# Kernel optimization log

Hardware: AMD Instinct MI355X
Metric: run time of the kernel (lower is better)

Reference implementation:

```python
import jax, jax.numpy as jnp
import numpy as np

T = 32  # simulation_length
L = 4   # number of NeuralCores in the chain


def to_uniform_spikes(x, cycle, sim_len):
    """Uniform spike encoding: emit round(x*T) spikes evenly spaced over T cycles.
    Faithful to SpikingUnifiedCoreFlow.to_uniform_spikes."""
    N = jnp.round(x * sim_len).astype(jnp.int32)
    mask = (N != 0) & (N != sim_len) & (cycle < sim_len)
    N_safe = jnp.maximum(N, 1)
    spacing = sim_len / N_safe.astype(x.dtype)          # T / N
    fire = mask & (jnp.floor(cycle / spacing) < N_safe) & (jnp.floor(jnp.mod(cycle, spacing)) == 0)
    out = fire.astype(x.dtype)
    return jnp.where(N == sim_len, jnp.ones_like(out), out)  # saturated channels fire every cycle


def setup_inputs() -> dict:
    key = jax.random.key(0)
    k0, k1 = jax.random.split(key)
    x = jax.random.uniform(k0, (128, 1024), dtype=jnp.float32)          # activations in [0,1]
    weights = jax.random.normal(k1, (L, 1024, 1024), dtype=jnp.float32) * 0.02  # (neurons, axons) per core
    thresholds = jnp.ones((L,), dtype=jnp.float32)
    return {"x": x, "weights": weights, "thresholds": thresholds}


def reference(x, weights, thresholds):
    """Rate-mode spiking simulation over a chain of NeuralCores.
    Per cycle: encode input to spikes (Uniform), propagate through cores with
    LIF integration (membrane += W @ spikes; spike = threshold < membrane;
    membrane -= spike * threshold), output = mean spike train of last core."""
    B = x.shape[0]
    H = weights.shape[1]

    def step(mem, cycle):
        sig = to_uniform_spikes(x, cycle, T)            # (B, axons_in)
        new_mems = []
        for l in range(L):
            m = mem[l] + sig @ weights[l].T             # F.linear(sig, W)
            s = (thresholds[l] < m).astype(x.dtype)     # thresholding_mode '<'
            m = m - s * thresholds[l]                   # Default firing: subtract reset
            new_mems.append(m)
            sig = s                                     # feed downstream core this cycle
        return jnp.stack(new_mems), sig                 # sig = last core spikes

    mem0 = jnp.zeros((L, B, H), dtype=x.dtype)
    _, out_spikes = jax.lax.scan(step, mem0, jnp.arange(T))  # (T, B, H)
    return out_spikes.mean(axis=0)                      # spike counts -> rates
```

## Files before the change

kernel.cpp:

```cpp
#include <hip/hip_runtime.h>
#include <stdint.h>


typedef __attribute__((ext_vector_type(4)))  int   i32x4;
typedef __attribute__((ext_vector_type(16))) int   i32x16;
typedef __attribute__((ext_vector_type(4)))  float f32x4;

#define SCALE_F 4294967296.0f
#define NSL 4

__device__ __forceinline__ void gload16(const void* g, void* l) {
    __builtin_amdgcn_global_load_lds(
        (const __attribute__((address_space(1))) void*)g,
        (__attribute__((address_space(3))) void*)l, 16, 0, 0);
}

__device__ __forceinline__ i32x4 expand16(unsigned int f) {
    i32x4 r;
    #pragma unroll
    for (int d = 0; d < 4; ++d)
        r[d] = (int)((((f >> (4 * d)) & 0xFu) * 0x00204081u) & 0x01010101u);
    return r;
}

__global__ void k_prep(const float* __restrict__ x, const float* __restrict__ w,
                       uint32_t* __restrict__ Am, signed char* __restrict__ planes) {
    if (blockIdx.x < 4096) {
        int tid = blockIdx.x * 256 + threadIdx.x;
        int l = tid >> 18;
        int rest4 = (tid & 0x3FFFF) << 2;
        f32x4 wv = *reinterpret_cast<const f32x4*>(w + ((size_t)l << 20) + rest4);
        long long q[4];
        #pragma unroll
        for (int i = 0; i < 4; ++i) q[i] = llrintf(wv[i] * SCALE_F);
        #pragma unroll
        for (int s = 0; s < NSL; ++s) {
            uint32_t pack = 0;
            #pragma unroll
            for (int i = 0; i < 4; ++i) {
                int d = (int)(signed char)((unsigned char)(q[i] & 255));
                q[i] = (q[i] - d) >> 8;
                pack |= ((uint32_t)(unsigned char)d) << (8 * i);
            }
            *reinterpret_cast<uint32_t*>(planes + (((size_t)(l * NSL + s)) << 20) + rest4) = pack;
        }
    } else {
        const int wid  = ((blockIdx.x - 4096) * 256 + threadIdx.x) >> 6;
        const int lane = threadIdx.x & 63;
        const int b = wid >> 4, kc = wid & 15;
        float v = x[b * 1024 + kc * 64 + lane];
        int N = (int)rintf(v * 32.0f);
        uint32_t bits = 0;
        if (N >= 32) {
            bits = 0xFFFFFFFFu;
        } else if (N > 0) {
            float spacing = 32.0f / (float)N;
            #pragma unroll
            for (int t = 0; t < 32; ++t) {
                float fm = fmodf((float)t, spacing);
                if (fm < 1.0f) bits |= (1u << t);
            }
        }
        uint32_t cap = 0;
        #pragma unroll
        for (int t = 0; t < 32; ++t) {
            unsigned long long bal = __ballot((bits >> t) & 1u);
            if (lane == t)      cap = (uint32_t)bal;
            if (lane == t + 32) cap = (uint32_t)(bal >> 32);
        }
        const int t = lane & 31, ww = lane >> 5;
        Am[(size_t)(b * 32 + t) * 32 + kc * 2 + ww] = cap;
    }
}

__global__ __launch_bounds__(512, 4) void k_fused(
        const uint32_t* __restrict__ Am,
        const signed char* __restrict__ planes,
        const float* __restrict__ th,
        uint32_t* __restrict__ AmNext,
        float* __restrict__ out,
        int layer) {
    __shared__ alignas(16) signed char lds[2][32768];

    const int tid  = threadIdx.x;
    const int lane = tid & 63;
    const int wave = tid >> 6;
    const int mw   = wave >> 1;
    const int nw   = wave & 1;
    const int lr   = lane & 31;
    const int hi   = lane >> 5;

    const int xc = blockIdx.x & 7, q = blockIdx.x >> 3;
    const int nTile = xc * 2 + (q & 1);
    const int mTile = q >> 1;
    const int mBase = mTile * 128, nBase = nTile * 64;

    const signed char* srcB[NSL];
    {
        const int r0 = tid >> 3, qs = tid & 7;
        const int sw0 = (qs ^ (r0 & 7)) * 16;
        #pragma unroll
        for (int s = 0; s < NSL; ++s)
            srcB[s] = planes + (((size_t)(layer * NSL + s)) << 20)
                    + (size_t)(nBase + r0) * 1024 + sw0;
    }
    const uint32_t* aRow = Am + (size_t)(mBase + mw * 32 + lr) * 32;

    int baddr[4];
    {
        const int brow = nw * 32 + lr;
        #pragma unroll
        for (int ks = 0; ks < 4; ++ks)
            baddr[ks] = brow * 128 + (((ks * 2 + hi) ^ (brow & 7)) * 16);
    }

    i32x16 acc[NSL];
    #pragma unroll
    for (int s = 0; s < NSL; ++s)
        #pragma unroll
        for (int r = 0; r < 16; ++r) acc[s][r] = 0;

    auto H0 = [&](int buf, int c) {
        const int ko = c * 128;
        gload16(srcB[0] + ko, &lds[buf][0]    + tid * 16);
        gload16(srcB[1] + ko, &lds[buf][8192] + tid * 16);
    };
    auto H1 = [&](int buf, int c) {
        const int ko = c * 128;
        gload16(srcB[2] + ko, &lds[buf][16384] + tid * 16);
        gload16(srcB[3] + ko, &lds[buf][24576] + tid * 16);
    };

    i32x4 amr[2];
    H0(0, 0);
    amr[0] = *reinterpret_cast<const i32x4*>(aRow);
    H1(0, 0);

    #pragma unroll
    for (int c = 0; c < 8; ++c) {
        const int buf = c & 1;
        const signed char* lb = &lds[buf][0];

        asm volatile("s_waitcnt vmcnt(2)" ::: "memory");
        __builtin_amdgcn_s_barrier();
        asm volatile("" ::: "memory");

        if (c + 1 < 8) {
            H0(buf ^ 1, c + 1);
            amr[(c + 1) & 1] = *reinterpret_cast<const i32x4*>(aRow + (c + 1) * 4);
            H1(buf ^ 1, c + 1);
        }

        i32x4 af[4];
        __builtin_amdgcn_s_setprio(1);
        #pragma unroll
        for (int ks = 0; ks < 4; ++ks) {
            af[ks] = expand16((((unsigned)amr[c & 1][ks]) >> (16 * hi)) & 0xFFFFu);
            #pragma unroll
            for (int s = 0; s < 2; ++s) {
                i32x4 bf = *reinterpret_cast<const i32x4*>(lb + s * 8192 + baddr[ks]);
                acc[s] = __builtin_amdgcn_mfma_i32_32x32x32_i8(af[ks], bf, acc[s], 0, 0, 0);
            }
        }
        __builtin_amdgcn_s_setprio(0);

        if (c + 1 < 8) asm volatile("s_waitcnt vmcnt(5)" ::: "memory");
        else           asm volatile("s_waitcnt vmcnt(0)" ::: "memory");
        __builtin_amdgcn_s_barrier();
        asm volatile("" ::: "memory");

        __builtin_amdgcn_s_setprio(1);
        #pragma unroll
        for (int ks = 0; ks < 4; ++ks) {
            #pragma unroll
            for (int s = 0; s < 2; ++s) {
                i32x4 bf = *reinterpret_cast<const i32x4*>(lb + (2 + s) * 8192 + baddr[ks]);
                acc[2 + s] = __builtin_amdgcn_mfma_i32_32x32x32_i8(af[ks], bf, acc[2 + s], 0, 0, 0);
            }
        }
        __builtin_amdgcn_s_setprio(0);
    }

    const long long TH = llrintf(th[layer] * SCALE_F);
    const int batch = mTile * 4 + mw;
    uint32_t bits = 0;
    long long mmem = 0;
    #pragma unroll
    for (int half = 0; half < 2; ++half) {
        long long own[8], par[8];
        #pragma unroll
        for (int r = 0; r < 8; ++r) {
            long long v = 0;
            #pragma unroll
            for (int s = 0; s < NSL; ++s)
                v += ((long long)acc[s][half * 8 + r]) << (8 * s);
            own[r] = v;
        }
        #pragma unroll
        for (int r = 0; r < 8; ++r) {
            int plo = __shfl((int)(uint32_t)own[r], lane ^ 32, 64);
            int phi = __shfl((int)(own[r] >> 32), lane ^ 32, 64);
            par[r] = ((long long)phi << 32) | (uint32_t)plo;
        }
        #pragma unroll
        for (int tq = 0; tq < 16; ++tq) {
            const int idx = (tq >> 3) * 4 + (tq & 3);
            const int usePar = ((tq >> 2) & 1) ^ hi;
            long long v = usePar ? par[idx] : own[idx];
            mmem += v;
            if (mmem > TH) { mmem -= TH; bits |= (1u << (half * 16 + tq)); }
        }
    }

    if (AmNext) {
        uint32_t cap = 0;
        #pragma unroll
        for (int t = 0; t < 32; ++t) {
            unsigned long long bal = __ballot((bits >> t) & 1u);
            if (lane == t) cap = (uint32_t)bal;
        }
        if (hi == 0)
            AmNext[(size_t)(batch * 32 + lr) * 32 + nTile * 2 + nw] = cap;
    } else if (hi == 0) {
        out[batch * 1024 + nBase + nw * 32 + lr] = (float)__popc(bits) * 0.03125f;
    }
}

extern "C" void kernel_launch(void* const* d_in, const int* in_sizes, int n_in,
                              void* d_out, int out_size, void* d_ws, size_t ws_size,
                              hipStream_t stream) {
    const float* x  = (const float*)d_in[0];
    const float* w  = (const float*)d_in[1];
    const float* th = (const float*)d_in[2];
    float* out = (float*)d_out;
    char* ws = (char*)d_ws;

    signed char* planes = (signed char*)(ws);
    uint32_t*    Am0    = (uint32_t*)(ws + 16777216);
    uint32_t*    Am1    = (uint32_t*)(ws + 17301504);

    k_prep<<<4608, 256, 0, stream>>>(x, w, Am0, planes);

    uint32_t* Ain = Am0;
    uint32_t* Anx = Am1;
    for (int l = 0; l < 4; ++l) {
        k_fused<<<512, 512, 0, stream>>>(Ain, planes, th,
                                         (l < 3) ? Anx : nullptr,
                                         (l == 3) ? out : nullptr, l);
        uint32_t* tmp = Ain; Ain = Anx; Anx = tmp;
    }
}
```

Before: 105.0 us.

## Register-block two M tiles per wave and halve block size in fused layer kernel

Blocks shrink from 8 to 4 waves. Each wave now computes two 32-row M tiles, so every B fragment read from LDS feeds two MFMAs. Each thread issues twice as many global-to-LDS loads, and the vmcnt waits are rescaled to the new load count per stage. This cuts LDS read traffic per MFMA and per-block overhead, at the cost of doubled accumulator registers and half as many waves per CU for latency hiding.

```diff
diff --git a/kernel.cpp b/kernel.cpp
--- a/kernel.cpp
+++ b/kernel.cpp
@@ -73,7 +73,7 @@
     }
 }
 
-__global__ __launch_bounds__(512, 4) void k_fused(
+__global__ __launch_bounds__(256, 2) void k_fused(
         const uint32_t* __restrict__ Am,
         const signed char* __restrict__ planes,
         const float* __restrict__ th,
@@ -104,7 +104,8 @@
             srcB[s] = planes + (((size_t)(layer * NSL + s)) << 20)
                     + (size_t)(nBase + r0) * 1024 + sw0;
     }
-    const uint32_t* aRow = Am + (size_t)(mBase + mw * 32 + lr) * 32;
+    const uint32_t* aRow0 = Am + (size_t)(mBase + mw * 64 + lr) * 32;
+    const uint32_t* aRow1 = aRow0 + 32 * 32;
 
     int baddr[4];
     {
@@ -114,26 +115,33 @@
             baddr[ks] = brow * 128 + (((ks * 2 + hi) ^ (brow & 7)) * 16);
     }
 
-    i32x16 acc[NSL];
-    #pragma unroll
-    for (int s = 0; s < NSL; ++s)
-        #pragma unroll
-        for (int r = 0; r < 16; ++r) acc[s][r] = 0;
+    i32x16 acc[2][NSL];
+    #pragma unroll
+    for (int m = 0; m < 2; ++m)
+        #pragma unroll
+        for (int s = 0; s < NSL; ++s)
+            #pragma unroll
+            for (int r = 0; r < 16; ++r) acc[m][s][r] = 0;
 
     auto H0 = [&](int buf, int c) {
         const int ko = c * 128;
-        gload16(srcB[0] + ko, &lds[buf][0]    + tid * 16);
-        gload16(srcB[1] + ko, &lds[buf][8192] + tid * 16);
+        gload16(srcB[0] + ko,         &lds[buf][0]     + tid * 16);
+        gload16(srcB[0] + ko + 32768, &lds[buf][4096]  + tid * 16);
+        gload16(srcB[1] + ko,         &lds[buf][8192]  + tid * 16);
+        gload16(srcB[1] + ko + 32768, &lds[buf][12288] + tid * 16);
     };
     auto H1 = [&](int buf, int c) {
         const int ko = c * 128;
-        gload16(srcB[2] + ko, &lds[buf][16384] + tid * 16);
-        gload16(srcB[3] + ko, &lds[buf][24576] + tid * 16);
+        gload16(srcB[2] + ko,         &lds[buf][16384] + tid * 16);
+        gload16(srcB[2] + ko + 32768, &lds[buf][20480] + tid * 16);
+        gload16(srcB[3] + ko,         &lds[buf][24576] + tid * 16);
+        gload16(srcB[3] + ko + 32768, &lds[buf][28672] + tid * 16);
     };
 
-    i32x4 amr[2];
+    i32x4 amr0[2], amr1[2];
     H0(0, 0);
-    amr[0] = *reinterpret_cast<const i32x4*>(aRow);
+    amr0[0] = *reinterpret_cast<const i32x4*>(aRow0);
+    amr1[0] = *reinterpret_cast<const i32x4*>(aRow1);
     H1(0, 0);
 
     #pragma unroll
@@ -141,30 +149,33 @@
         const int buf = c & 1;
         const signed char* lb = &lds[buf][0];
 
-        asm volatile("s_waitcnt vmcnt(2)" ::: "memory");
+        asm volatile("s_waitcnt vmcnt(4)" ::: "memory");
         __builtin_amdgcn_s_barrier();
         asm volatile("" ::: "memory");
 
         if (c + 1 < 8) {
             H0(buf ^ 1, c + 1);
-            amr[(c + 1) & 1] = *reinterpret_cast<const i32x4*>(aRow + (c + 1) * 4);
+            amr0[(c + 1) & 1] = *reinterpret_cast<const i32x4*>(aRow0 + (c + 1) * 4);
+            amr1[(c + 1) & 1] = *reinterpret_cast<const i32x4*>(aRow1 + (c + 1) * 4);
             H1(buf ^ 1, c + 1);
         }
 
-        i32x4 af[4];
+        i32x4 af0[4], af1[4];
         __builtin_amdgcn_s_setprio(1);
         #pragma unroll
         for (int ks = 0; ks < 4; ++ks) {
-            af[ks] = expand16((((unsigned)amr[c & 1][ks]) >> (16 * hi)) & 0xFFFFu);
-            #pragma unroll
-            for (int s = 0; s < 2; ++s) {
-                i32x4 bf = *reinterpret_cast<const i32x4*>(lb + s * 8192 + baddr[ks]);
-                acc[s] = __builtin_amdgcn_mfma_i32_32x32x32_i8(af[ks], bf, acc[s], 0, 0, 0);
-            }
+            af0[ks] = expand16((((unsigned)amr0[c & 1][ks]) >> (16 * hi)) & 0xFFFFu);
+            af1[ks] = expand16((((unsigned)amr1[c & 1][ks]) >> (16 * hi)) & 0xFFFFu);
+            i32x4 bf0 = *reinterpret_cast<const i32x4*>(lb + 0 * 8192 + baddr[ks]);
+            i32x4 bf1 = *reinterpret_cast<const i32x4*>(lb + 1 * 8192 + baddr[ks]);
+            acc[0][0] = __builtin_amdgcn_mfma_i32_32x32x32_i8(af0[ks], bf0, acc[0][0], 0, 0, 0);
+            acc[1][0] = __builtin_amdgcn_mfma_i32_32x32x32_i8(af1[ks], bf0, acc[1][0], 0, 0, 0);
+            acc[0][1] = __builtin_amdgcn_mfma_i32_32x32x32_i8(af0[ks], bf1, acc[0][1], 0, 0, 0);
+            acc[1][1] = __builtin_amdgcn_mfma_i32_32x32x32_i8(af1[ks], bf1, acc[1][1], 0, 0, 0);
         }
         __builtin_amdgcn_s_setprio(0);
 
-        if (c + 1 < 8) asm volatile("s_waitcnt vmcnt(5)" ::: "memory");
+        if (c + 1 < 8) asm volatile("s_waitcnt vmcnt(10)" ::: "memory");
         else           asm volatile("s_waitcnt vmcnt(0)" ::: "memory");
         __builtin_amdgcn_s_barrier();
         asm volatile("" ::: "memory");
@@ -172,57 +183,61 @@
         __builtin_amdgcn_s_setprio(1);
         #pragma unroll
         for (int ks = 0; ks < 4; ++ks) {
-            #pragma unroll
-            for (int s = 0; s < 2; ++s) {
-                i32x4 bf = *reinterpret_cast<const i32x4*>(lb + (2 + s) * 8192 + baddr[ks]);
-                acc[2 + s] = __builtin_amdgcn_mfma_i32_32x32x32_i8(af[ks], bf, acc[2 + s], 0, 0, 0);
-            }
+            i32x4 bf2 = *reinterpret_cast<const i32x4*>(lb + 2 * 8192 + baddr[ks]);
+            i32x4 bf3 = *reinterpret_cast<const i32x4*>(lb + 3 * 8192 + baddr[ks]);
+            acc[0][2] = __builtin_amdgcn_mfma_i32_32x32x32_i8(af0[ks], bf2, acc[0][2], 0, 0, 0);
+            acc[1][2] = __builtin_amdgcn_mfma_i32_32x32x32_i8(af1[ks], bf2, acc[1][2], 0, 0, 0);
+            acc[0][3] = __builtin_amdgcn_mfma_i32_32x32x32_i8(af0[ks], bf3, acc[0][3], 0, 0, 0);
+            acc[1][3] = __builtin_amdgcn_mfma_i32_32x32x32_i8(af1[ks], bf3, acc[1][3], 0, 0, 0);
         }
         __builtin_amdgcn_s_setprio(0);
     }
 
     const long long TH = llrintf(th[layer] * SCALE_F);
-    const int batch = mTile * 4 + mw;
-    uint32_t bits = 0;
-    long long mmem = 0;
-    #pragma unroll
-    for (int half = 0; half < 2; ++half) {
-        long long own[8], par[8];
-        #pragma unroll
-        for (int r = 0; r < 8; ++r) {
-            long long v = 0;
-            #pragma unroll
-            for (int s = 0; s < NSL; ++s)
-                v += ((long long)acc[s][half * 8 + r]) << (8 * s);
-            own[r] = v;
-        }
-        #pragma unroll
-        for (int r = 0; r < 8; ++r) {
-            int plo = __shfl((int)(uint32_t)own[r], lane ^ 32, 64);
-            int phi = __shfl((int)(own[r] >> 32), lane ^ 32, 64);
-            par[r] = ((long long)phi << 32) | (uint32_t)plo;
-        }
-        #pragma unroll
-        for (int tq = 0; tq < 16; ++tq) {
-            const int idx = (tq >> 3) * 4 + (tq & 3);
-            const int usePar = ((tq >> 2) & 1) ^ hi;
-            long long v = usePar ? par[idx] : own[idx];
-            mmem += v;
-            if (mmem > TH) { mmem -= TH; bits |= (1u << (half * 16 + tq)); }
-        }
-    }
-
-    if (AmNext) {
-        uint32_t cap = 0;
-        #pragma unroll
-        for (int t = 0; t < 32; ++t) {
-            unsigned long long bal = __ballot((bits >> t) & 1u);
-            if (lane == t) cap = (uint32_t)bal;
-        }
-        if (hi == 0)
-            AmNext[(size_t)(batch * 32 + lr) * 32 + nTile * 2 + nw] = cap;
-    } else if (hi == 0) {
-        out[batch * 1024 + nBase + nw * 32 + lr] = (float)__popc(bits) * 0.03125f;
+    #pragma unroll
+    for (int m = 0; m < 2; ++m) {
+        const int batch = mTile * 4 + mw * 2 + m;
+        uint32_t bits = 0;
+        long long mmem = 0;
+        #pragma unroll
+        for (int half = 0; half < 2; ++half) {
+            long long own[8], par[8];
+            #pragma unroll
+            for (int r = 0; r < 8; ++r) {
+                long long v = 0;
+                #pragma unroll
+                for (int s = 0; s < NSL; ++s)
+                    v += ((long long)acc[m][s][half * 8 + r]) << (8 * s);
+                own[r] = v;
+            }
+            #pragma unroll
+            for (int r = 0; r < 8; ++r) {
+                int plo = __shfl((int)(uint32_t)own[r], lane ^ 32, 64);
+                int phi = __shfl((int)(own[r] >> 32), lane ^ 32, 64);
+                par[r] = ((long long)phi << 32) | (uint32_t)plo;
+            }
+            #pragma unroll
+            for (int tq = 0; tq < 16; ++tq) {
+                const int idx = (tq >> 3) * 4 + (tq & 3);
+                const int usePar = ((tq >> 2) & 1) ^ hi;
+                long long v = usePar ? par[idx] : own[idx];
+                mmem += v;
+                if (mmem > TH) { mmem -= TH; bits |= (1u << (half * 16 + tq)); }
+            }
+        }
+
+        if (AmNext) {
+            uint32_t cap = 0;
+            #pragma unroll
+            for (int t = 0; t < 32; ++t) {
+                unsigned long long bal = __ballot((bits >> t) & 1u);
+                if (lane == t) cap = (uint32_t)bal;
+            }
+            if (hi == 0)
+                AmNext[(size_t)(batch * 32 + lr) * 32 + nTile * 2 + nw] = cap;
+        } else if (hi == 0) {
+            out[batch * 1024 + nBase + nw * 32 + lr] = (float)__popc(bits) * 0.03125f;
+        }
     }
 }
 
@@ -244,7 +259,7 @@
     uint32_t* Ain = Am0;
     uint32_t* Anx = Am1;
     for (int l = 0; l < 4; ++l) {
-        k_fused<<<512, 512, 0, stream>>>(Ain, planes, th,
+        k_fused<<<512, 256, 0, stream>>>(Ain, planes, th,
                                          (l < 3) ? Anx : nullptr,
                                          (l == 3) ? out : nullptr, l);
         uint32_t* tmp = Ain; Ain = Anx; Anx = tmp;
```

After: 105.0 us. Within noise of the previous version (+0.1%).

## Fuse four layer launches into one persistent kernel with grid barrier

Applied to the files above, without the earlier changes.

Replaces the four per-layer kernel launches with one persistent kernel that loops over layers and synchronises all 512 blocks through an atomic-counter grid barrier. The next layer's first weight-plane tile is prefetched into LDS before the barrier, so it overlaps the spike epilogue and the wait. This removes the launch gaps and kernel-boundary drains between layers. In exchange it assumes all 512 blocks are co-resident, or the spin barrier deadlocks. It also adds spinning atomic traffic and leaves AmIn un-qualified by restrict.

```diff
diff --git a/kernel.cpp b/kernel.cpp
--- a/kernel.cpp
+++ b/kernel.cpp
@@ -24,7 +24,9 @@
 }
 
 __global__ void k_prep(const float* __restrict__ x, const float* __restrict__ w,
-                       uint32_t* __restrict__ Am, signed char* __restrict__ planes) {
+                       uint32_t* __restrict__ Am, signed char* __restrict__ planes,
+                       unsigned* __restrict__ bar) {
+    if (blockIdx.x == 0 && threadIdx.x == 0) *bar = 0;
     if (blockIdx.x < 4096) {
         int tid = blockIdx.x * 256 + threadIdx.x;
         int l = tid >> 18;
@@ -73,13 +75,22 @@
     }
 }
 
-__global__ __launch_bounds__(512, 4) void k_fused(
-        const uint32_t* __restrict__ Am,
+__device__ __forceinline__ void grid_sync(unsigned* bar, unsigned target) {
+    __syncthreads();
+    if (threadIdx.x == 0) {
+        __hip_atomic_fetch_add(bar, 1u, __ATOMIC_RELEASE, __HIP_MEMORY_SCOPE_AGENT);
+        while (__hip_atomic_load(bar, __ATOMIC_ACQUIRE, __HIP_MEMORY_SCOPE_AGENT) < target)
+            __builtin_amdgcn_s_sleep(2);
+    }
+    __syncthreads();
+}
+
+__global__ __launch_bounds__(512, 4) void k_fused_all(
         const signed char* __restrict__ planes,
         const float* __restrict__ th,
-        uint32_t* __restrict__ AmNext,
+        uint32_t* Am0, uint32_t* Am1,
         float* __restrict__ out,
-        int layer) {
+        unsigned* __restrict__ bar) {
     __shared__ alignas(16) signed char lds[2][32768];
 
     const int tid  = threadIdx.x;
@@ -101,10 +112,9 @@
         const int sw0 = (qs ^ (r0 & 7)) * 16;
         #pragma unroll
         for (int s = 0; s < NSL; ++s)
-            srcB[s] = planes + (((size_t)(layer * NSL + s)) << 20)
+            srcB[s] = planes + ((size_t)s << 20)
                     + (size_t)(nBase + r0) * 1024 + sw0;
     }
-    const uint32_t* aRow = Am + (size_t)(mBase + mw * 32 + lr) * 32;
 
     int baddr[4];
     {
@@ -113,12 +123,6 @@
         for (int ks = 0; ks < 4; ++ks)
             baddr[ks] = brow * 128 + (((ks * 2 + hi) ^ (brow & 7)) * 16);
     }
-
-    i32x16 acc[NSL];
-    #pragma unroll
-    for (int s = 0; s < NSL; ++s)
-        #pragma unroll
-        for (int r = 0; r < 16; ++r) acc[s][r] = 0;
 
     auto H0 = [&](int buf, int c) {
         const int ko = c * 128;
@@ -131,98 +135,121 @@
         gload16(srcB[3] + ko, &lds[buf][24576] + tid * 16);
     };
 
-    i32x4 amr[2];
-    H0(0, 0);
-    amr[0] = *reinterpret_cast<const i32x4*>(aRow);
-    H1(0, 0);
-
-    #pragma unroll
-    for (int c = 0; c < 8; ++c) {
-        const int buf = c & 1;
-        const signed char* lb = &lds[buf][0];
-
-        asm volatile("s_waitcnt vmcnt(2)" ::: "memory");
-        __builtin_amdgcn_s_barrier();
-        asm volatile("" ::: "memory");
-
-        if (c + 1 < 8) {
-            H0(buf ^ 1, c + 1);
-            amr[(c + 1) & 1] = *reinterpret_cast<const i32x4*>(aRow + (c + 1) * 4);
-            H1(buf ^ 1, c + 1);
-        }
-
-        i32x4 af[4];
-        __builtin_amdgcn_s_setprio(1);
-        #pragma unroll
-        for (int ks = 0; ks < 4; ++ks) {
-            af[ks] = expand16((((unsigned)amr[c & 1][ks]) >> (16 * hi)) & 0xFFFFu);
-            #pragma unroll
-            for (int s = 0; s < 2; ++s) {
-                i32x4 bf = *reinterpret_cast<const i32x4*>(lb + s * 8192 + baddr[ks]);
-                acc[s] = __builtin_amdgcn_mfma_i32_32x32x32_i8(af[ks], bf, acc[s], 0, 0, 0);
-            }
-        }
-        __builtin_amdgcn_s_setprio(0);
-
-        if (c + 1 < 8) asm volatile("s_waitcnt vmcnt(5)" ::: "memory");
-        else           asm volatile("s_waitcnt vmcnt(0)" ::: "memory");
-        __builtin_amdgcn_s_barrier();
-        asm volatile("" ::: "memory");
-
-        __builtin_amdgcn_s_setprio(1);
-        #pragma unroll
-        for (int ks = 0; ks < 4; ++ks) {
-            #pragma unroll
-            for (int s = 0; s < 2; ++s) {
-                i32x4 bf = *reinterpret_cast<const i32x4*>(lb + (2 + s) * 8192 + baddr[ks]);
-                acc[2 + s] = __builtin_amdgcn_mfma_i32_32x32x32_i8(af[ks], bf, acc[2 + s], 0, 0, 0);
-            }
-        }
-        __builtin_amdgcn_s_setprio(0);
-    }
-
-    const long long TH = llrintf(th[layer] * SCALE_F);
-    const int batch = mTile * 4 + mw;
-    uint32_t bits = 0;
-    long long mmem = 0;
-    #pragma unroll
-    for (int half = 0; half < 2; ++half) {
-        long long own[8], par[8];
-        #pragma unroll
-        for (int r = 0; r < 8; ++r) {
-            long long v = 0;
-            #pragma unroll
-            for (int s = 0; s < NSL; ++s)
-                v += ((long long)acc[s][half * 8 + r]) << (8 * s);
-            own[r] = v;
-        }
-        #pragma unroll
-        for (int r = 0; r < 8; ++r) {
-            int plo = __shfl((int)(uint32_t)own[r], lane ^ 32, 64);
-            int phi = __shfl((int)(own[r] >> 32), lane ^ 32, 64);
-            par[r] = ((long long)phi << 32) | (uint32_t)plo;
-        }
-        #pragma unroll
-        for (int tq = 0; tq < 16; ++tq) {
-            const int idx = (tq >> 3) * 4 + (tq & 3);
-            const int usePar = ((tq >> 2) & 1) ^ hi;
-            long long v = usePar ? par[idx] : own[idx];
-            mmem += v;
-            if (mmem > TH) { mmem -= TH; bits |= (1u << (half * 16 + tq)); }
-        }
-    }
-
-    if (AmNext) {
-        uint32_t cap = 0;
-        #pragma unroll
-        for (int t = 0; t < 32; ++t) {
-            unsigned long long bal = __ballot((bits >> t) & 1u);
-            if (lane == t) cap = (uint32_t)bal;
-        }
-        if (hi == 0)
-            AmNext[(size_t)(batch * 32 + lr) * 32 + nTile * 2 + nw] = cap;
-    } else if (hi == 0) {
-        out[batch * 1024 + nBase + nw * 32 + lr] = (float)__popc(bits) * 0.03125f;
+    uint32_t* AmIn  = Am0;
+    uint32_t* AmOut = Am1;
+
+    #pragma unroll 1
+    for (int layer = 0; layer < 4; ++layer) {
+        const uint32_t* aRow = AmIn + (size_t)(mBase + mw * 32 + lr) * 32;
+
+        if (layer == 0) H0(0, 0);
+        i32x4 amr[2];
+        amr[0] = *reinterpret_cast<const i32x4*>(aRow);
+        H1(0, 0);
+
+        i32x16 acc[NSL];
+        #pragma unroll
+        for (int s = 0; s < NSL; ++s)
+            #pragma unroll
+            for (int r = 0; r < 16; ++r) acc[s][r] = 0;
+
+        #pragma unroll
+        for (int c = 0; c < 8; ++c) {
+            const int buf = c & 1;
+            const signed char* lb = &lds[buf][0];
+
+            asm volatile("s_waitcnt vmcnt(2)" ::: "memory");
+            __builtin_amdgcn_s_barrier();
+            asm volatile("" ::: "memory");
+
+            if (c + 1 < 8) {
+                H0(buf ^ 1, c + 1);
+                amr[(c + 1) & 1] = *reinterpret_cast<const i32x4*>(aRow + (c + 1) * 4);
+                H1(buf ^ 1, c + 1);
+            }
+
+            i32x4 af[4];
+            __builtin_amdgcn_s_setprio(1);
+            #pragma unroll
+            for (int ks = 0; ks < 4; ++ks) {
+                af[ks] = expand16((((unsigned)amr[c & 1][ks]) >> (16 * hi)) & 0xFFFFu);
+                #pragma unroll
+                for (int s = 0; s < 2; ++s) {
+                    i32x4 bf = *reinterpret_cast<const i32x4*>(lb + s * 8192 + baddr[ks]);
+                    acc[s] = __builtin_amdgcn_mfma_i32_32x32x32_i8(af[ks], bf, acc[s], 0, 0, 0);
+                }
+            }
+            __builtin_amdgcn_s_setprio(0);
+
+            if (c + 1 < 8) asm volatile("s_waitcnt vmcnt(5)" ::: "memory");
+            else           asm volatile("s_waitcnt vmcnt(0)" ::: "memory");
+            __builtin_amdgcn_s_barrier();
+            asm volatile("" ::: "memory");
+
+            __builtin_amdgcn_s_setprio(1);
+            #pragma unroll
+            for (int ks = 0; ks < 4; ++ks) {
+                #pragma unroll
+                for (int s = 0; s < 2; ++s) {
+                    i32x4 bf = *reinterpret_cast<const i32x4*>(lb + (2 + s) * 8192 + baddr[ks]);
+                    acc[2 + s] = __builtin_amdgcn_mfma_i32_32x32x32_i8(af[ks], bf, acc[2 + s], 0, 0, 0);
+                }
+            }
+            __builtin_amdgcn_s_setprio(0);
+        }
+
+        if (layer < 3) {
+            #pragma unroll
+            for (int s = 0; s < NSL; ++s) srcB[s] += (size_t)NSL << 20;
+            H0(0, 0);
+        }
+
+        const long long TH = llrintf(th[layer] * SCALE_F);
+        const int batch = mTile * 4 + mw;
+        uint32_t bits = 0;
+        long long mmem = 0;
+        #pragma unroll
+        for (int half = 0; half < 2; ++half) {
+            long long own[8], par[8];
+            #pragma unroll
+            for (int r = 0; r < 8; ++r) {
+                long long v = 0;
+                #pragma unroll
+                for (int s = 0; s < NSL; ++s)
+                    v += ((long long)acc[s][half * 8 + r]) << (8 * s);
+                own[r] = v;
+            }
+            #pragma unroll
+            for (int r = 0; r < 8; ++r) {
+                int plo = __shfl((int)(uint32_t)own[r], lane ^ 32, 64);
+                int phi = __shfl((int)(own[r] >> 32), lane ^ 32, 64);
+                par[r] = ((long long)phi << 32) | (uint32_t)plo;
+            }
+            #pragma unroll
+            for (int tq = 0; tq < 16; ++tq) {
+                const int idx = (tq >> 3) * 4 + (tq & 3);
+                const int usePar = ((tq >> 2) & 1) ^ hi;
+                long long v = usePar ? par[idx] : own[idx];
+                mmem += v;
+                if (mmem > TH) { mmem -= TH; bits |= (1u << (half * 16 + tq)); }
+            }
+        }
+
+        if (layer < 3) {
+            uint32_t cap = 0;
+            #pragma unroll
+            for (int t = 0; t < 32; ++t) {
+                unsigned long long bal = __ballot((bits >> t) & 1u);
+                if (lane == t) cap = (uint32_t)bal;
+            }
+            if (hi == 0)
+                AmOut[(size_t)(batch * 32 + lr) * 32 + nTile * 2 + nw] = cap;
+
+            grid_sync(bar, 512u * (unsigned)(layer + 1));
+            uint32_t* tmp = AmIn; AmIn = AmOut; AmOut = tmp;
+        } else if (hi == 0) {
+            out[batch * 1024 + nBase + nw * 32 + lr] = (float)__popc(bits) * 0.03125f;
+        }
     }
 }
 
@@ -238,15 +265,8 @@
     signed char* planes = (signed char*)(ws);
     uint32_t*    Am0    = (uint32_t*)(ws + 16777216);
     uint32_t*    Am1    = (uint32_t*)(ws + 17301504);
-
-    k_prep<<<4608, 256, 0, stream>>>(x, w, Am0, planes);
-
-    uint32_t* Ain = Am0;
-    uint32_t* Anx = Am1;
-    for (int l = 0; l < 4; ++l) {
-        k_fused<<<512, 512, 0, stream>>>(Ain, planes, th,
-                                         (l < 3) ? Anx : nullptr,
-                                         (l == 3) ? out : nullptr, l);
-        uint32_t* tmp = Ain; Ain = Anx; Anx = tmp;
-    }
-}
+    unsigned*    bar    = (unsigned*)(ws + 17825792);
+
+    k_prep<<<4608, 256, 0, stream>>>(x, w, Am0, planes, bar);
+    k_fused_all<<<512, 512, 0, stream>>>(planes, th, Am0, Am1, out, bar);
+}
```

Measured after the change: 221.6 us. 2.11x slower.

## Store weight byte-planes in k-chunk-major layout for conflict-free LDS reads

Applied to the files above, without the earlier changes.

The prep kernel now has each thread quantize 16 consecutive weights and write 16-byte packed groups into a layout where each 16-byte k-group is stored contiguously across all rows (g*16384 + row*16). The fused GEMM kernel's global-to-LDS loads and LDS read addresses are changed to match, replacing the XOR swizzle with plain k-group-major addressing. The aim is fewer, wider prep stores and simpler LDS addressing that stays free of bank conflicts. In exchange, each global load in the GEMM now strides 128 KB between chunks, and prep loads fewer but wider vectors per thread.

```diff
diff --git a/kernel.cpp b/kernel.cpp
--- a/kernel.cpp
+++ b/kernel.cpp
@@ -25,27 +25,42 @@
 
 __global__ void k_prep(const float* __restrict__ x, const float* __restrict__ w,
                        uint32_t* __restrict__ Am, signed char* __restrict__ planes) {
-    if (blockIdx.x < 4096) {
+    if (blockIdx.x < 1024) {
         int tid = blockIdx.x * 256 + threadIdx.x;
-        int l = tid >> 18;
-        int rest4 = (tid & 0x3FFFF) << 2;
-        f32x4 wv = *reinterpret_cast<const f32x4*>(w + ((size_t)l << 20) + rest4);
-        long long q[4];
-        #pragma unroll
-        for (int i = 0; i < 4; ++i) q[i] = llrintf(wv[i] * SCALE_F);
+        int l    = tid >> 16;
+        int rest = tid & 0xFFFF;
+        int row  = rest >> 6;
+        int g    = rest & 63;
+        const float* wp = w + ((size_t)l << 20) + (size_t)row * 1024 + g * 16;
+        long long q[16];
+        #pragma unroll
+        for (int i = 0; i < 16; i += 4) {
+            f32x4 wv = *reinterpret_cast<const f32x4*>(wp + i);
+            q[i + 0] = llrintf(wv[0] * SCALE_F);
+            q[i + 1] = llrintf(wv[1] * SCALE_F);
+            q[i + 2] = llrintf(wv[2] * SCALE_F);
+            q[i + 3] = llrintf(wv[3] * SCALE_F);
+        }
         #pragma unroll
         for (int s = 0; s < NSL; ++s) {
-            uint32_t pack = 0;
-            #pragma unroll
-            for (int i = 0; i < 4; ++i) {
-                int d = (int)(signed char)((unsigned char)(q[i] & 255));
-                q[i] = (q[i] - d) >> 8;
-                pack |= ((uint32_t)(unsigned char)d) << (8 * i);
-            }
-            *reinterpret_cast<uint32_t*>(planes + (((size_t)(l * NSL + s)) << 20) + rest4) = pack;
+            i32x4 pk;
+            #pragma unroll
+            for (int e = 0; e < 4; ++e) {
+                uint32_t pack = 0;
+                #pragma unroll
+                for (int i = 0; i < 4; ++i) {
+                    int idx = e * 4 + i;
+                    int d = (int)(signed char)((unsigned char)(q[idx] & 255));
+                    q[idx] = (q[idx] - d) >> 8;
+                    pack |= ((uint32_t)(unsigned char)d) << (8 * i);
+                }
+                pk[e] = (int)pack;
+            }
+            *reinterpret_cast<i32x4*>(planes + (((size_t)(l * NSL + s)) << 20)
+                                      + (size_t)g * 16384 + row * 16) = pk;
         }
     } else {
-        const int wid  = ((blockIdx.x - 4096) * 256 + threadIdx.x) >> 6;
+        const int wid  = ((blockIdx.x - 1024) * 256 + threadIdx.x) >> 6;
         const int lane = threadIdx.x & 63;
         const int b = wid >> 4, kc = wid & 15;
         float v = x[b * 1024 + kc * 64 + lane];
@@ -97,12 +112,12 @@
 
     const signed char* srcB[NSL];
     {
-        const int r0 = tid >> 3, qs = tid & 7;
-        const int sw0 = (qs ^ (r0 & 7)) * 16;
+        const int ks0 = tid >> 6;
+        const int rr  = tid & 63;
         #pragma unroll
         for (int s = 0; s < NSL; ++s)
             srcB[s] = planes + (((size_t)(layer * NSL + s)) << 20)
-                    + (size_t)(nBase + r0) * 1024 + sw0;
+                    + (size_t)ks0 * 16384 + (size_t)(nBase + rr) * 16;
     }
     const uint32_t* aRow = Am + (size_t)(mBase + mw * 32 + lr) * 32;
 
@@ -111,7 +126,7 @@
         const int brow = nw * 32 + lr;
         #pragma unroll
         for (int ks = 0; ks < 4; ++ks)
-            baddr[ks] = brow * 128 + (((ks * 2 + hi) ^ (brow & 7)) * 16);
+            baddr[ks] = (ks * 2 + hi) * 1024 + brow * 16;
     }
 
     i32x16 acc[NSL];
@@ -121,12 +136,12 @@
         for (int r = 0; r < 16; ++r) acc[s][r] = 0;
 
     auto H0 = [&](int buf, int c) {
-        const int ko = c * 128;
+        const int ko = c * 131072;
         gload16(srcB[0] + ko, &lds[buf][0]    + tid * 16);
         gload16(srcB[1] + ko, &lds[buf][8192] + tid * 16);
     };
     auto H1 = [&](int buf, int c) {
-        const int ko = c * 128;
+        const int ko = c * 131072;
         gload16(srcB[2] + ko, &lds[buf][16384] + tid * 16);
         gload16(srcB[3] + ko, &lds[buf][24576] + tid * 16);
     };
@@ -239,7 +254,7 @@
     uint32_t*    Am0    = (uint32_t*)(ws + 16777216);
     uint32_t*    Am1    = (uint32_t*)(ws + 17301504);
 
-    k_prep<<<4608, 256, 0, stream>>>(x, w, Am0, planes);
+    k_prep<<<1536, 256, 0, stream>>>(x, w, Am0, planes);
 
     uint32_t* Ain = Am0;
     uint32_t* Anx = Am1;
```

Result: slower. 107.9 us (+2.8%).
